# Performance work log

Measured on AMD Instinct MI355X. Metric: run time of the kernel, lower is better.

## Reference

```python
import jax, jax.numpy as jnp
import numpy as np

N = 100000   # nodes
E = 1600000  # edges (avg degree 16)
D = 128      # input feature dim
H = 64       # hidden dim (hard-coded in Sage.__init__)
C = 40       # output classes


def setup_inputs() -> dict:
    key = jax.random.key(0)
    ks = jax.random.split(key, 9)
    s_in = 1.0 / np.sqrt(D)
    s_h = 1.0 / np.sqrt(H)
    return {
        "x": jax.random.normal(ks[0], (N, D), jnp.float32),
        "edge_index": jax.random.randint(ks[1], (2, E), 0, N, dtype=jnp.int64),
        # SAGEConv params: lin_l acts on aggregated neighbors (carries bias),
        # lin_r acts on the root/self features (no bias), per PyG defaults.
        "W1_l": jax.random.uniform(ks[2], (D, H), jnp.float32, -s_in, s_in),
        "W1_r": jax.random.uniform(ks[3], (D, H), jnp.float32, -s_in, s_in),
        "b1": jax.random.uniform(ks[4], (H,), jnp.float32, -s_in, s_in),
        "W2_l": jax.random.uniform(ks[5], (H, C), jnp.float32, -s_h, s_h),
        "W2_r": jax.random.uniform(ks[6], (H, C), jnp.float32, -s_h, s_h),
        "b2": jax.random.uniform(ks[7], (C,), jnp.float32, -s_h, s_h),
    }


def _sage_conv(x, src, dst, W_l, W_r, b):
    # mean-aggregate neighbor features at destination nodes
    msg = x[src]                                             # [E, F] gather
    summed = jax.ops.segment_sum(msg, dst, num_segments=N)   # [N, F]
    deg = jax.ops.segment_sum(jnp.ones((src.shape[0],), x.dtype), dst,
                              num_segments=N)                # [N]
    agg = summed / jnp.maximum(deg, 1.0)[:, None]
    return agg @ W_l + x @ W_r + b


def reference(x, edge_index, W1_l, W1_r, b1, W2_l, W2_r, b2):
    src, dst = edge_index[0], edge_index[1]
    h = _sage_conv(x, src, dst, W1_l, W1_r, b1)
    h = jax.nn.relu(h)
    # F.dropout(training=False) in eval mode -> identity
    out = _sage_conv(h, src, dst, W2_l, W2_r, b2)
    return jax.nn.log_softmax(out, axis=1)
```

## Files before the change

### kernel.cpp

```cpp
#include <hip/hip_runtime.h>

__device__ __forceinline__ float bf2f(unsigned short u) {
  union { unsigned int i; float f; } c; c.i = ((unsigned int)u) << 16; return c.f;
}
__device__ __forceinline__ unsigned short f2bf(float f) {
  union { float f; unsigned int i; } c; c.f = f;
  unsigned int x = c.i;
  return (unsigned short)((x + 0x7fffu + ((x >> 16) & 1u)) >> 16);
}
__device__ __forceinline__ float lo16(unsigned int w) { return bf2f((unsigned short)(w & 0xffffu)); }
__device__ __forceinline__ float hi16(unsigned int w) { return bf2f((unsigned short)(w >> 16)); }

#define DD 128
#define HH 64
#define CC 40
#define NBUCK 512
#define NCHUNK 128
#define MAXNPB 256
#define NQ 4
#define NR 4

using bf16x8 = __attribute__((ext_vector_type(8))) short;
using f32x4  = __attribute__((ext_vector_type(4))) float;

__global__ __launch_bounds__(256) void detect_prepw(
    const unsigned int* e32, const unsigned int* x32, int* flags,
    const void* W1l, const void* W1r, const void* b1,
    const void* W2l, const void* W2r, const void* b2,
    unsigned short* Wb1, unsigned short* Wb2, float* b1f, float* b2f) {
  int tid = threadIdx.x;
  if (blockIdx.x == 0) {
    __shared__ unsigned int redOr[256];
    __shared__ int redCnt[256];
    unsigned int v = 0;
    for (int i = tid; i < 4096; i += 256) v |= e32[2 * i + 1];
    int cnt = 0;
    for (int i = tid; i < 4096; i += 256) {
      unsigned int w = x32[i];
      unsigned int expo = (w >> 7) & 0xffu;
      unsigned short lo = (unsigned short)(w & 0xffffu);
      if (lo == 0 || (expo >= 100u && expo <= 133u)) cnt++;
    }
    redOr[tid] = v; redCnt[tid] = cnt; __syncthreads();
    for (int s = 128; s > 0; s >>= 1) {
      if (tid < s) { redOr[tid] |= redOr[tid + s]; redCnt[tid] += redCnt[tid + s]; }
      __syncthreads();
    }
    if (tid == 0) {
      flags[0] = (redOr[0] == 0u) ? 1 : 0;
      flags[1] = (redCnt[0] < 2048) ? 1 : 0;
    }
    return;
  }
  __shared__ int red[256];
  const unsigned int* w32 = (const unsigned int*)W1l;
  int cnt = 0;
  for (int i = tid; i < 4096; i += 256) {
    unsigned int w = w32[i];
    unsigned int expo = (w >> 7) & 0xffu;
    unsigned short lo = (unsigned short)(w & 0xffffu);
    if (lo == 0 || (expo >= 100u && expo <= 133u)) cnt++;
  }
  red[tid] = cnt; __syncthreads();
  for (int s = 128; s > 0; s >>= 1) {
    if (tid < s) red[tid] += red[tid + s];
    __syncthreads();
  }
  int isf = (red[0] < 2048) ? 1 : 0;
  auto rd = [&](const void* p, int i) -> float {
    return isf ? ((const float*)p)[i] : bf2f(((const unsigned short*)p)[i]);
  };
  if (blockIdx.x == 1) {
    for (int idx = tid; idx < 128 * 128; idx += 256) {
      int n = idx >> 7, k = idx & 127;
      float v = (n < HH) ? rd(W1l, k * HH + n) : rd(W1r, k * HH + (n - HH));
      Wb1[idx] = f2bf(v);
    }
  } else {
    for (int idx = tid; idx < 48 * 128; idx += 256) {
      int n = idx >> 7, k = idx & 127;
      float v = 0.f;
      if (n < CC) v = (k < HH) ? rd(W2l, k * CC + n) : rd(W2r, (k - HH) * CC + n);
      Wb2[idx] = f2bf(v);
    }
    if (tid < HH) b1f[tid] = rd(b1, tid);
    if (tid < CC) b2f[tid] = rd(b2, tid);
  }
}

__global__ __launch_bounds__(256) void hist_or_t1(
    const int* e32, int E, int N, const int* flags, int nodesPerB, int* histG,
    const void* xraw, const unsigned short* Wb1, const float* b1f,
    unsigned short* t1, unsigned short* s1, int T1B) {
  __shared__ int cnt[NBUCK * NR];
  int b = blockIdx.x;
  int tid = threadIdx.x;

  if (b < NCHUNK) {
    for (int i = tid; i < NBUCK * NR; i += 256) cnt[i] = 0;
    __syncthreads();
    int isI64 = flags[0];
    int rep = tid & (NR - 1);
    int chunk = (E + NCHUNK - 1) / NCHUNK;
    int e0 = b * chunk, e1 = min(e0 + chunk, E);
    for (int i = e0 + tid; i < e1; i += 256) {
      int d = isI64 ? e32[2 * (E + i)] : e32[E + i];
      d = min(max(d, 0), N - 1);
      atomicAdd(&cnt[(d / nodesPerB) * NR + rep], 1);
    }
    __syncthreads();
    for (int i = tid; i < NBUCK; i += 256)
      histG[i * NCHUNK + b] =
          cnt[i * NR] + cnt[i * NR + 1] + cnt[i * NR + 2] + cnt[i * NR + 3];
    return;
  }

  int t = b - NCHUNK;
  if (t >= T1B) return;
  int lane = tid & 63, wv = tid >> 6;
  int nb = t * 64 + wv * 16;
  int oc = lane & 15, kgrp = lane >> 4;
  int node = min(nb + oc, N - 1);
  f32x4 acc[8];
#pragma unroll
  for (int i = 0; i < 8; i++) acc[i] = (f32x4){0.f, 0.f, 0.f, 0.f};

  if (flags[1]) {
    const float4* x4 = (const float4*)xraw;
#pragma unroll
    for (int kb = 0; kb < 4; kb++) {
      int k0 = kb * 32 + kgrp * 8;
      float4 a0 = x4[(size_t)node * 32 + (k0 >> 2)];
      float4 a1 = x4[(size_t)node * 32 + (k0 >> 2) + 1];
      bf16x8 af;
      af[0] = (short)f2bf(a0.x); af[1] = (short)f2bf(a0.y);
      af[2] = (short)f2bf(a0.z); af[3] = (short)f2bf(a0.w);
      af[4] = (short)f2bf(a1.x); af[5] = (short)f2bf(a1.y);
      af[6] = (short)f2bf(a1.z); af[7] = (short)f2bf(a1.w);
#pragma unroll
      for (int nblk = 0; nblk < 8; nblk++) {
        bf16x8 bfr = *(const bf16x8*)&Wb1[(nblk * 16 + oc) * 128 + k0];
        acc[nblk] = __builtin_amdgcn_mfma_f32_16x16x32_bf16(af, bfr, acc[nblk], 0, 0, 0);
      }
    }
  } else {
    const unsigned short* x16 = (const unsigned short*)xraw;
#pragma unroll
    for (int kb = 0; kb < 4; kb++) {
      int k0 = kb * 32 + kgrp * 8;
      bf16x8 af = *(const bf16x8*)&x16[(size_t)node * 128 + k0];
#pragma unroll
      for (int nblk = 0; nblk < 8; nblk++) {
        bf16x8 bfr = *(const bf16x8*)&Wb1[(nblk * 16 + oc) * 128 + k0];
        acc[nblk] = __builtin_amdgcn_mfma_f32_16x16x32_bf16(af, bfr, acc[nblk], 0, 0, 0);
      }
    }
  }

  int r0 = kgrp * 4;
#pragma unroll
  for (int nblk = 0; nblk < 8; nblk++) {
    float bias = (nblk >= 4) ? b1f[(nblk - 4) * 16 + oc] : 0.f;
#pragma unroll
    for (int r = 0; r < 4; r++) {
      int nn = nb + r0 + r;
      if (nn < N) {
        if (nblk < 4)
          t1[(size_t)nn * HH + nblk * 16 + oc] = f2bf(acc[nblk][r]);
        else
          s1[(size_t)nn * HH + (nblk - 4) * 16 + oc] = f2bf(acc[nblk][r] + bias);
      }
    }
  }
}

__global__ __launch_bounds__(128) void scanA(const int* histG, int* ohist, int* bsum) {
  __shared__ int t[NCHUNK];
  int b = blockIdx.x, tid = threadIdx.x;
  int v = histG[b * NCHUNK + tid];
  t[tid] = v; __syncthreads();
  for (int st = 1; st < NCHUNK; st <<= 1) {
    int u = (tid >= st) ? t[tid - st] : 0;
    __syncthreads();
    t[tid] += u;
    __syncthreads();
  }
  ohist[b * NCHUNK + tid] = t[tid] - v;
  if (tid == NCHUNK - 1) bsum[b] = t[tid];
}

__global__ __launch_bounds__(512) void scanB(const int* bsum, int* bbase,
                                             int* row_ptr4, int N, int E) {
  __shared__ int t[NBUCK];
  int tid = threadIdx.x;
  int v = bsum[tid];
  t[tid] = v; __syncthreads();
  for (int st = 1; st < NBUCK; st <<= 1) {
    int u = (tid >= st) ? t[tid - st] : 0;
    __syncthreads();
    t[tid] += u;
    __syncthreads();
  }
  bbase[tid] = t[tid] - v;
  if (tid == 0) { bbase[NBUCK] = E; row_ptr4[NQ * N] = E; }
}

__global__ __launch_bounds__(256) void scatter_k(const int* e32, int E, int N,
                                                 const int* flags, int nodesPerB,
                                                 const int* ohist, const int* bbase,
                                                 uint2* ebuf) {
  __shared__ int cur[NBUCK];
  int tid = threadIdx.x;
  for (int i = tid; i < NBUCK; i += 256)
    cur[i] = ohist[i * NCHUNK + blockIdx.x] + bbase[i];
  __syncthreads();
  int isI64 = flags[0];
  int chunk = (E + NCHUNK - 1) / NCHUNK;
  int e0 = blockIdx.x * chunk, e1 = min(e0 + chunk, E);
  for (int i = e0 + tid; i < e1; i += 256) {
    int s, d;
    if (isI64) { s = e32[2 * i]; d = e32[2 * (E + i)]; }
    else       { s = e32[i];     d = e32[E + i]; }
    s = min(max(s, 0), N - 1);
    d = min(max(d, 0), N - 1);
    int p = atomicAdd(&cur[d / nodesPerB], 1);
    ebuf[p] = make_uint2((unsigned)s, (unsigned)d);
  }
}

__global__ __launch_bounds__(256) void bktB(
    const uint2* ebuf, const int* bbase,
    int nodesPerB, int qshift, int* row_ptr4, float* invd, int* col, int N) {
  __shared__ int cnt[MAXNPB * NQ];
  __shared__ int sA[256];
  int b = blockIdx.x;
  int tid = threadIdx.x;
  int base_node = b * nodesPerB;
  int nn = min(nodesPerB, N - base_node);
  if (nn <= 0) return;
  int nk = nn * NQ;
  int eb0 = bbase[b], eb1 = bbase[b + 1];
  int nE = eb1 - eb0;
  const uint2* ee = ebuf + eb0;
  for (int i = tid; i < nk; i += 256) cnt[i] = 0;
  __syncthreads();
  for (int i = tid; i < nE; i += 256) {
    uint2 eg = ee[i];
    int key = ((int)eg.y - base_node) * NQ + (int)(eg.x >> qshift);
    atomicAdd(&cnt[key], 1);
  }
  __syncthreads();
  for (int i = tid; i < nn; i += 256) {
    int d = cnt[NQ * i] + cnt[NQ * i + 1] + cnt[NQ * i + 2] + cnt[NQ * i + 3];
    invd[base_node + i] = 1.0f / (float)max(d, 1);
  }
  __syncthreads();
  int per = (nk + 255) / 256;
  int myb = tid * per;
  int dreg[4];
  int ssum = 0;
#pragma unroll
  for (int k = 0; k < 4; k++) {
    int idx = myb + k;
    int v = (k < per && idx < nk) ? cnt[idx] : 0;
    dreg[k] = v; ssum += v;
  }
  sA[tid] = ssum;
  __syncthreads();
  for (int st = 1; st < 256; st <<= 1) {
    int t = (tid >= st) ? sA[tid - st] : 0;
    __syncthreads();
    sA[tid] += t;
    __syncthreads();
  }
  int run = eb0 + sA[tid] - ssum;
  __syncthreads();
#pragma unroll
  for (int k = 0; k < 4; k++) {
    int idx = myb + k;
    if (k < per && idx < nk) {
      row_ptr4[(size_t)(base_node + (idx >> 2)) * NQ + (idx & 3)] = run;
      cnt[idx] = run;
      run += dreg[k];
    }
  }
  __syncthreads();
  for (int i = tid; i < nE; i += 256) {
    uint2 eg = ee[i];
    int key = ((int)eg.y - base_node) * NQ + (int)(eg.x >> qshift);
    int p = atomicAdd(&cnt[key], 1);
    col[p] = (int)eg.x;
  }
}

__device__ __forceinline__ void gather_seg(const uint4* t8, const int* col,
                                           int s0, int s1, int r, int c,
                                           float acc[8]) {
  for (int base = s0; base < s1; base += 4) {
    int i = base + r;
    bool g = (i < s1);
    int nb = g ? col[i] : 0;
    uint4 v = make_uint4(0, 0, 0, 0);
    if (g) v = t8[(size_t)nb * 8 + c];
    acc[0] += lo16(v.x); acc[1] += hi16(v.x);
    acc[2] += lo16(v.y); acc[3] += hi16(v.y);
    acc[4] += lo16(v.z); acc[5] += hi16(v.z);
    acc[6] += lo16(v.w); acc[7] += hi16(v.w);
  }
}

__global__ __launch_bounds__(256) void aggregate1(const unsigned short* t1,
                                                  const unsigned short* s1,
                                                  const int* row_ptr4, const float* invd,
                                                  const int* col, unsigned short* h, int N) {
  int wave = threadIdx.x >> 6, lane = threadIdx.x & 63;
  int ns = lane >> 5, r = (lane >> 3) & 3, c = lane & 7;
  int n = blockIdx.x * 8 + wave * 2 + ns;
  if (n >= N) return;
  int4 rp = *(const int4*)&row_ptr4[(size_t)NQ * n];
  int e4 = row_ptr4[(size_t)NQ * n + 4];
  float acc[8] = {0, 0, 0, 0, 0, 0, 0, 0};
  const uint4* t8 = (const uint4*)t1;
  gather_seg(t8, col, rp.x, rp.y, r, c, acc);
  gather_seg(t8, col, rp.y, rp.z, r, c, acc);
  gather_seg(t8, col, rp.z, rp.w, r, c, acc);
  gather_seg(t8, col, rp.w, e4, r, c, acc);
#pragma unroll
  for (int m = 8; m <= 16; m <<= 1)
#pragma unroll
    for (int i = 0; i < 8; i++) acc[i] += __shfl_xor(acc[i], m, 64);

  if (r == 0) {
    float id = invd[n];
    uint4 sv = ((const uint4*)s1)[(size_t)n * 8 + c];
    float s[8] = {lo16(sv.x), hi16(sv.x), lo16(sv.y), hi16(sv.y),
                  lo16(sv.z), hi16(sv.z), lo16(sv.w), hi16(sv.w)};
    unsigned int o[4];
#pragma unroll
    for (int i = 0; i < 4; i++) {
      float a0 = fmaxf(acc[2 * i] * id + s[2 * i], 0.f);
      float a1 = fmaxf(acc[2 * i + 1] * id + s[2 * i + 1], 0.f);
      o[i] = (unsigned int)f2bf(a0) | ((unsigned int)f2bf(a1) << 16);
    }
    ((uint4*)h)[(size_t)n * 8 + c] = make_uint4(o[0], o[1], o[2], o[3]);
  }
}

__global__ __launch_bounds__(256) void agg2(const unsigned short* h,
                                            const int* row_ptr4, const float* invd,
                                            const int* col, unsigned short* aggh, int N) {
  int wave = threadIdx.x >> 6, lane = threadIdx.x & 63;
  int ns = lane >> 5, r = (lane >> 3) & 3, c = lane & 7;
  int n = blockIdx.x * 8 + wave * 2 + ns;
  if (n >= N) return;
  int4 rp = *(const int4*)&row_ptr4[(size_t)NQ * n];
  int e4 = row_ptr4[(size_t)NQ * n + 4];
  float acc[8] = {0, 0, 0, 0, 0, 0, 0, 0};
  const uint4* h8 = (const uint4*)h;
  gather_seg(h8, col, rp.x, rp.y, r, c, acc);
  gather_seg(h8, col, rp.y, rp.z, r, c, acc);
  gather_seg(h8, col, rp.z, rp.w, r, c, acc);
  gather_seg(h8, col, rp.w, e4, r, c, acc);
#pragma unroll
  for (int m = 8; m <= 16; m <<= 1)
#pragma unroll
    for (int i = 0; i < 8; i++) acc[i] += __shfl_xor(acc[i], m, 64);

  if (r == 0) {
    float id = invd[n];
    unsigned int o[4];
#pragma unroll
    for (int i = 0; i < 4; i++) {
      o[i] = (unsigned int)f2bf(acc[2 * i] * id) |
             ((unsigned int)f2bf(acc[2 * i + 1] * id) << 16);
    }
    ((uint4*)aggh)[(size_t)n * 8 + c] = make_uint4(o[0], o[1], o[2], o[3]);
  }
}

__global__ __launch_bounds__(256) void final_k(const unsigned short* aggh,
                                               const unsigned short* h,
                                               const unsigned short* Wb2,
                                               const float* b2f,
                                               float* out, int N) {
  int tid = threadIdx.x;
  int lane = tid & 63, wv = tid >> 6;
  int nb = blockIdx.x * 64 + wv * 16;
  int oc = lane & 15, kgrp = lane >> 4;
  int node = min(nb + oc, N - 1);
  f32x4 acc[3];
#pragma unroll
  for (int i = 0; i < 3; i++) acc[i] = (f32x4){0.f, 0.f, 0.f, 0.f};

#pragma unroll
  for (int kb = 0; kb < 4; kb++) {
    int k0 = kb * 32 + kgrp * 8;
    const unsigned short* src = (kb < 2) ? aggh : h;
    int kk = k0 & 63;
    bf16x8 af = *(const bf16x8*)&src[(size_t)node * HH + kk];
#pragma unroll
    for (int nblk = 0; nblk < 3; nblk++) {
      bf16x8 bfr = *(const bf16x8*)&Wb2[(nblk * 16 + oc) * 128 + k0];
      acc[nblk] = __builtin_amdgcn_mfma_f32_16x16x32_bf16(af, bfr, acc[nblk], 0, 0, 0);
    }
  }

#pragma unroll
  for (int nblk = 0; nblk < 3; nblk++) {
    int cc = nblk * 16 + oc;
    float bias = (cc < CC) ? b2f[cc] : 0.f;
#pragma unroll
    for (int r = 0; r < 4; r++) acc[nblk][r] += bias;
  }

#pragma unroll
  for (int r = 0; r < 4; r++) {
    int nn = nb + kgrp * 4 + r;
    float m = -INFINITY;
#pragma unroll
    for (int nblk = 0; nblk < 3; nblk++)
      if (nblk * 16 + oc < CC) m = fmaxf(m, acc[nblk][r]);
    for (int off = 1; off <= 8; off <<= 1) m = fmaxf(m, __shfl_xor(m, off, 64));
    float s = 0.f;
#pragma unroll
    for (int nblk = 0; nblk < 3; nblk++)
      if (nblk * 16 + oc < CC) s += __expf(acc[nblk][r] - m);
    for (int off = 1; off <= 8; off <<= 1) s += __shfl_xor(s, off, 64);
    float lse = m + __logf(s);
    if (nn < N) {
#pragma unroll
      for (int nblk = 0; nblk < 3; nblk++) {
        int cc = nblk * 16 + oc;
        if (cc < CC) out[(size_t)nn * CC + cc] = acc[nblk][r] - lse;
      }
    }
  }
}

extern "C" void kernel_launch(void* const* d_in, const int* in_sizes, int n_in,
                              void* d_out, int out_size, void* d_ws, size_t ws_size,
                              hipStream_t stream) {
  const void* x   = d_in[0];
  const int*  e   = (const int*)d_in[1];
  const void* W1l = d_in[2];
  const void* W1r = d_in[3];
  const void* b1  = d_in[4];
  const void* W2l = d_in[5];
  const void* W2r = d_in[6];
  const void* b2  = d_in[7];
  float* out = (float*)d_out;

  const int N = in_sizes[0] / DD;
  const int E = in_sizes[1] / 2;
  const int nodesPerB = (N + NBUCK - 1) / NBUCK;
  const int nbuck = (N + nodesPerB - 1) / nodesPerB;
  const int T1B = (N + 63) / 64;
  int qshift = 0;
  while (((unsigned)(N - 1) >> qshift) > 3u) qshift++;

  char* w = (char*)d_ws;
  size_t off = 0;
  auto carve = [&](size_t bytes) -> void* {
    void* p = (void*)(w + off);
    off += (bytes + 255) & ~(size_t)255;
    return p;
  };
  int* col      = (int*)carve((size_t)E * 4);
  int* row_ptr4 = (int*)carve(((size_t)N * NQ + 1) * 4);
  float* invd   = (float*)carve((size_t)N * 4);
  int* histG    = (int*)carve((size_t)NBUCK * NCHUNK * 4);
  int* ohist    = (int*)carve((size_t)NBUCK * NCHUNK * 4);
  int* bsum     = (int*)carve(NBUCK * 4);
  int* bbase    = (int*)carve((NBUCK + 1) * 4);
  int* flags    = (int*)carve(8);
  unsigned short* t1   = (unsigned short*)carve((size_t)N * HH * 2);
  unsigned short* s1   = (unsigned short*)carve((size_t)N * HH * 2);
  unsigned short* h    = (unsigned short*)carve((size_t)N * HH * 2);
  unsigned short* Wb1  = (unsigned short*)carve(128 * 128 * 2);
  unsigned short* Wb2  = (unsigned short*)carve(48 * 128 * 2);
  float* b1f   = (float*)carve(HH * sizeof(float));
  float* b2f   = (float*)carve(CC * sizeof(float));
  uint2* ebuf  = (uint2*)carve((size_t)E * 8);
  unsigned short* aggh = (unsigned short*)ebuf;
  (void)ws_size; (void)n_in; (void)out_size;

  detect_prepw<<<3, 256, 0, stream>>>((const unsigned int*)e, (const unsigned int*)x,
                                      flags, W1l, W1r, b1, W2l, W2r, b2,
                                      Wb1, Wb2, b1f, b2f);
  hist_or_t1<<<NCHUNK + T1B, 256, 0, stream>>>(e, E, N, flags, nodesPerB, histG,
                                               x, Wb1, b1f, t1, s1, T1B);
  scanA<<<NBUCK, 128, 0, stream>>>(histG, ohist, bsum);
  scanB<<<1, 512, 0, stream>>>(bsum, bbase, row_ptr4, N, E);
  scatter_k<<<NCHUNK, 256, 0, stream>>>(e, E, N, flags, nodesPerB, ohist, bbase, ebuf);
  bktB<<<nbuck, 256, 0, stream>>>(ebuf, bbase, nodesPerB, qshift,
                                  row_ptr4, invd, col, N);
  aggregate1<<<(N + 7) / 8, 256, 0, stream>>>(t1, s1, row_ptr4, invd, col, h, N);
  agg2<<<(N + 7) / 8, 256, 0, stream>>>(h, row_ptr4, invd, col, aggh, N);
  final_k<<<(N + 63) / 64, 256, 0, stream>>>(aggh, h, Wb2, b2f, out, N);
}
```

Measured before the change: 316.1 us.

## Pack edges into 32-bit keys, cache bucket edges in LDS, fuse agg2 with final

```diff
diff --git a/kernel.cpp b/kernel.cpp
--- a/kernel.cpp
+++ b/kernel.cpp
@@ -19,6 +19,7 @@
 #define MAXNPB 256
 #define NQ 4
 #define NR 4
+#define ECAP 6144
 
 using bf16x8 = __attribute__((ext_vector_type(8))) short;
 using f32x4  = __attribute__((ext_vector_type(4))) float;
@@ -207,8 +208,9 @@
 
 __global__ __launch_bounds__(256) void scatter_k(const int* e32, int E, int N,
                                                  const int* flags, int nodesPerB,
+                                                 int qshift,
                                                  const int* ohist, const int* bbase,
-                                                 uint2* ebuf) {
+                                                 unsigned* ebuf) {
   __shared__ int cur[NBUCK];
   int tid = threadIdx.x;
   for (int i = tid; i < NBUCK; i += 256)
@@ -223,14 +225,18 @@
     else       { s = e32[i];     d = e32[E + i]; }
     s = min(max(s, 0), N - 1);
     d = min(max(d, 0), N - 1);
-    int p = atomicAdd(&cur[d / nodesPerB], 1);
-    ebuf[p] = make_uint2((unsigned)s, (unsigned)d);
+    int bk = d / nodesPerB;
+    int ld = d - bk * nodesPerB;
+    unsigned q = (unsigned)s >> qshift;
+    int p = atomicAdd(&cur[bk], 1);
+    ebuf[p] = ((unsigned)ld << 19) | (q << 17) | (unsigned)s;
   }
 }
 
 __global__ __launch_bounds__(256) void bktB(
-    const uint2* ebuf, const int* bbase,
-    int nodesPerB, int qshift, int* row_ptr4, float* invd, int* col, int N) {
+    const unsigned* ebuf, const int* bbase,
+    int nodesPerB, int* row_ptr4, float* invd, int* col, int N) {
+  __shared__ unsigned ecache[ECAP];
   __shared__ int cnt[MAXNPB * NQ];
   __shared__ int sA[256];
   int b = blockIdx.x;
@@ -241,13 +247,18 @@
   int nk = nn * NQ;
   int eb0 = bbase[b], eb1 = bbase[b + 1];
   int nE = eb1 - eb0;
-  const uint2* ee = ebuf + eb0;
+  const unsigned* ee = ebuf + eb0;
+  bool useL = (nE <= ECAP);
   for (int i = tid; i < nk; i += 256) cnt[i] = 0;
   __syncthreads();
-  for (int i = tid; i < nE; i += 256) {
-    uint2 eg = ee[i];
-    int key = ((int)eg.y - base_node) * NQ + (int)(eg.x >> qshift);
-    atomicAdd(&cnt[key], 1);
+  if (useL) {
+    for (int i = tid; i < nE; i += 256) {
+      unsigned v = ee[i];
+      ecache[i] = v;
+      atomicAdd(&cnt[v >> 17], 1);
+    }
+  } else {
+    for (int i = tid; i < nE; i += 256) atomicAdd(&cnt[ee[i] >> 17], 1);
   }
   __syncthreads();
   for (int i = tid; i < nn; i += 256) {
@@ -285,11 +296,18 @@
     }
   }
   __syncthreads();
-  for (int i = tid; i < nE; i += 256) {
-    uint2 eg = ee[i];
-    int key = ((int)eg.y - base_node) * NQ + (int)(eg.x >> qshift);
-    int p = atomicAdd(&cnt[key], 1);
-    col[p] = (int)eg.x;
+  if (useL) {
+    for (int i = tid; i < nE; i += 256) {
+      unsigned v = ecache[i];
+      int p = atomicAdd(&cnt[v >> 17], 1);
+      col[p] = (int)(v & 0x1FFFFu);
+    }
+  } else {
+    for (int i = tid; i < nE; i += 256) {
+      unsigned v = ee[i];
+      int p = atomicAdd(&cnt[v >> 17], 1);
+      col[p] = (int)(v & 0x1FFFFu);
+    }
   }
 }
 
@@ -346,62 +364,73 @@
   }
 }
 
-__global__ __launch_bounds__(256) void agg2(const unsigned short* h,
-                                            const int* row_ptr4, const float* invd,
-                                            const int* col, unsigned short* aggh, int N) {
-  int wave = threadIdx.x >> 6, lane = threadIdx.x & 63;
+__global__ __launch_bounds__(256) void agg2f(const unsigned short* h,
+                                             const int* row_ptr4, const float* invd,
+                                             const int* col,
+                                             const unsigned short* Wb2,
+                                             const float* b2f,
+                                             float* out, int N) {
+  __shared__ unsigned lds[64 * 33];
+  int tid = threadIdx.x, wv = tid >> 6, lane = tid & 63;
   int ns = lane >> 5, r = (lane >> 3) & 3, c = lane & 7;
-  int n = blockIdx.x * 8 + wave * 2 + ns;
-  if (n >= N) return;
-  int4 rp = *(const int4*)&row_ptr4[(size_t)NQ * n];
-  int e4 = row_ptr4[(size_t)NQ * n + 4];
-  float acc[8] = {0, 0, 0, 0, 0, 0, 0, 0};
+  int nb = blockIdx.x * 64;
   const uint4* h8 = (const uint4*)h;
-  gather_seg(h8, col, rp.x, rp.y, r, c, acc);
-  gather_seg(h8, col, rp.y, rp.z, r, c, acc);
-  gather_seg(h8, col, rp.z, rp.w, r, c, acc);
-  gather_seg(h8, col, rp.w, e4, r, c, acc);
-#pragma unroll
-  for (int m = 8; m <= 16; m <<= 1)
-#pragma unroll
-    for (int i = 0; i < 8; i++) acc[i] += __shfl_xor(acc[i], m, 64);
-
-  if (r == 0) {
-    float id = invd[n];
-    unsigned int o[4];
-#pragma unroll
-    for (int i = 0; i < 4; i++) {
-      o[i] = (unsigned int)f2bf(acc[2 * i] * id) |
-             ((unsigned int)f2bf(acc[2 * i + 1] * id) << 16);
-    }
-    ((uint4*)aggh)[(size_t)n * 8 + c] = make_uint4(o[0], o[1], o[2], o[3]);
-  }
-}
-
-__global__ __launch_bounds__(256) void final_k(const unsigned short* aggh,
-                                               const unsigned short* h,
-                                               const unsigned short* Wb2,
-                                               const float* b2f,
-                                               float* out, int N) {
-  int tid = threadIdx.x;
-  int lane = tid & 63, wv = tid >> 6;
-  int nb = blockIdx.x * 64 + wv * 16;
+
+  for (int rr = 0; rr < 8; rr++) {
+    int ln = wv * 16 + rr * 2 + ns;
+    int n = nb + ln;
+    float acc[8] = {0, 0, 0, 0, 0, 0, 0, 0};
+    int4 rp; int e4;
+    if (n < N) {
+      rp = *(const int4*)&row_ptr4[(size_t)NQ * n];
+      e4 = row_ptr4[(size_t)NQ * n + 4];
+    } else {
+      rp = make_int4(0, 0, 0, 0); e4 = 0;
+    }
+    gather_seg(h8, col, rp.x, rp.y, r, c, acc);
+    gather_seg(h8, col, rp.y, rp.z, r, c, acc);
+    gather_seg(h8, col, rp.z, rp.w, r, c, acc);
+    gather_seg(h8, col, rp.w, e4, r, c, acc);
+#pragma unroll
+    for (int m = 8; m <= 16; m <<= 1)
+#pragma unroll
+      for (int i = 0; i < 8; i++) acc[i] += __shfl_xor(acc[i], m, 64);
+    if (r == 0) {
+      float id = (n < N) ? invd[n] : 0.f;
+#pragma unroll
+      for (int q = 0; q < 4; q++) {
+        unsigned u = (unsigned)f2bf(acc[2 * q] * id) |
+                     ((unsigned)f2bf(acc[2 * q + 1] * id) << 16);
+        lds[ln * 33 + c * 4 + q] = u;
+      }
+    }
+  }
+  __syncthreads();
+
   int oc = lane & 15, kgrp = lane >> 4;
-  int node = min(nb + oc, N - 1);
-  f32x4 acc[3];
-#pragma unroll
-  for (int i = 0; i < 3; i++) acc[i] = (f32x4){0.f, 0.f, 0.f, 0.f};
+  int noderow = wv * 16 + oc;
+  int node = min(nb + noderow, N - 1);
+  f32x4 acc3[3];
+#pragma unroll
+  for (int i = 0; i < 3; i++) acc3[i] = (f32x4){0.f, 0.f, 0.f, 0.f};
 
 #pragma unroll
   for (int kb = 0; kb < 4; kb++) {
     int k0 = kb * 32 + kgrp * 8;
-    const unsigned short* src = (kb < 2) ? aggh : h;
-    int kk = k0 & 63;
-    bf16x8 af = *(const bf16x8*)&src[(size_t)node * HH + kk];
+    bf16x8 af;
+    if (kb < 2) {
+      union { unsigned u[4]; bf16x8 v; } cv;
+      int base = noderow * 33 + (k0 >> 1);
+      cv.u[0] = lds[base]; cv.u[1] = lds[base + 1];
+      cv.u[2] = lds[base + 2]; cv.u[3] = lds[base + 3];
+      af = cv.v;
+    } else {
+      af = *(const bf16x8*)&h[(size_t)node * HH + (k0 - 64)];
+    }
 #pragma unroll
     for (int nblk = 0; nblk < 3; nblk++) {
       bf16x8 bfr = *(const bf16x8*)&Wb2[(nblk * 16 + oc) * 128 + k0];
-      acc[nblk] = __builtin_amdgcn_mfma_f32_16x16x32_bf16(af, bfr, acc[nblk], 0, 0, 0);
+      acc3[nblk] = __builtin_amdgcn_mfma_f32_16x16x32_bf16(af, bfr, acc3[nblk], 0, 0, 0);
     }
   }
 
@@ -410,28 +439,28 @@
     int cc = nblk * 16 + oc;
     float bias = (cc < CC) ? b2f[cc] : 0.f;
 #pragma unroll
-    for (int r = 0; r < 4; r++) acc[nblk][r] += bias;
-  }
-
-#pragma unroll
-  for (int r = 0; r < 4; r++) {
-    int nn = nb + kgrp * 4 + r;
+    for (int rg = 0; rg < 4; rg++) acc3[nblk][rg] += bias;
+  }
+
+#pragma unroll
+  for (int rg = 0; rg < 4; rg++) {
+    int nn = nb + wv * 16 + kgrp * 4 + rg;
     float m = -INFINITY;
 #pragma unroll
     for (int nblk = 0; nblk < 3; nblk++)
-      if (nblk * 16 + oc < CC) m = fmaxf(m, acc[nblk][r]);
+      if (nblk * 16 + oc < CC) m = fmaxf(m, acc3[nblk][rg]);
     for (int off = 1; off <= 8; off <<= 1) m = fmaxf(m, __shfl_xor(m, off, 64));
     float s = 0.f;
 #pragma unroll
     for (int nblk = 0; nblk < 3; nblk++)
-      if (nblk * 16 + oc < CC) s += __expf(acc[nblk][r] - m);
+      if (nblk * 16 + oc < CC) s += __expf(acc3[nblk][rg] - m);
     for (int off = 1; off <= 8; off <<= 1) s += __shfl_xor(s, off, 64);
     float lse = m + __logf(s);
     if (nn < N) {
 #pragma unroll
       for (int nblk = 0; nblk < 3; nblk++) {
         int cc = nblk * 16 + oc;
-        if (cc < CC) out[(size_t)nn * CC + cc] = acc[nblk][r] - lse;
+        if (cc < CC) out[(size_t)nn * CC + cc] = acc3[nblk][rg] - lse;
       }
     }
   }
@@ -480,8 +509,7 @@
   unsigned short* Wb2  = (unsigned short*)carve(48 * 128 * 2);
   float* b1f   = (float*)carve(HH * sizeof(float));
   float* b2f   = (float*)carve(CC * sizeof(float));
-  uint2* ebuf  = (uint2*)carve((size_t)E * 8);
-  unsigned short* aggh = (unsigned short*)ebuf;
+  unsigned* ebuf = (unsigned*)carve((size_t)E * 4);
   (void)ws_size; (void)n_in; (void)out_size;
 
   detect_prepw<<<3, 256, 0, stream>>>((const unsigned int*)e, (const unsigned int*)x,
@@ -491,10 +519,9 @@
                                                x, Wb1, b1f, t1, s1, T1B);
   scanA<<<NBUCK, 128, 0, stream>>>(histG, ohist, bsum);
   scanB<<<1, 512, 0, stream>>>(bsum, bbase, row_ptr4, N, E);
-  scatter_k<<<NCHUNK, 256, 0, stream>>>(e, E, N, flags, nodesPerB, ohist, bbase, ebuf);
-  bktB<<<nbuck, 256, 0, stream>>>(ebuf, bbase, nodesPerB, qshift,
-                                  row_ptr4, invd, col, N);
+  scatter_k<<<NCHUNK, 256, 0, stream>>>(e, E, N, flags, nodesPerB, qshift,
+                                        ohist, bbase, ebuf);
+  bktB<<<nbuck, 256, 0, stream>>>(ebuf, bbase, nodesPerB, row_ptr4, invd, col, N);
   aggregate1<<<(N + 7) / 8, 256, 0, stream>>>(t1, s1, row_ptr4, invd, col, h, N);
-  agg2<<<(N + 7) / 8, 256, 0, stream>>>(h, row_ptr4, invd, col, aggh, N);
-  final_k<<<(N + 63) / 64, 256, 0, stream>>>(aggh, h, Wb2, b2f, out, N);
-}
+  agg2f<<<(N + 63) / 64, 256, 0, stream>>>(h, row_ptr4, invd, col, Wb2, b2f, out, N);
+}
```

After: 311.3 us. Within noise of the previous version (-1.5%).
